# Kernel tuning notes

Hardware: AMD Instinct MI355X
Metric: run time of the kernel (lower is better)

## Reference

```python
import jax, jax.numpy as jnp
import numpy as np

N, F, H, OUT, DDIM, E = 200000, 64, 256, 16, 768, 3200000


def setup_inputs() -> dict:
    key = jax.random.key(0)
    ks = jax.random.split(key, 20)
    s = lambda i, shp, sc=0.05: (jax.random.normal(ks[i], shp, jnp.float32) * sc)
    return dict(
        x=jax.random.normal(ks[0], (N, F), jnp.float32),
        edge_index=jax.random.randint(ks[1], (2, E), 0, N, dtype=jnp.int32),
        doc_feature=jax.random.normal(ks[2], (DDIM,), jnp.float32),
        pool_w=s(3, (F,)),
        init_weight=s(4, (F, F)),
        gru_w_ih=s(5, (3 * F, F)), gru_w_hh=s(6, (3 * F, F)),
        gru_b_ih=s(7, (3 * F,)), gru_b_hh=s(8, (3 * F,)),
        gnn_fc_w=s(9, (H, F)), gnn_fc_b=s(10, (H,)),
        doc_fc_w=s(11, (H, DDIM)), doc_fc_b=s(12, (H,)),
        ln_g=jnp.ones((2 * H,), jnp.float32), ln_b=jnp.zeros((2 * H,), jnp.float32),
        fusion_w=s(13, (H, 2 * H)), fusion_b=s(14, (H,)),
        task_w=s(15, (OUT, H)), task_b=s(16, (OUT,)),
        time_w=s(17, (1, H)), time_b=s(18, (1,)),
    )


def _forward(x, doc_feature, pool_w, init_weight, gru_w_ih, gru_w_hh, gru_b_ih,
             gru_b_hh, gnn_fc_w, gnn_fc_b, doc_fc_w, doc_fc_b, ln_g, ln_b,
             fusion_w, fusion_b, task_w, task_b, time_w, time_b, edge_index):
    n, f = x.shape
    # --- EvolveGCNH: TopK pooling, k = f since ratio = in_channels/num_nodes ---
    score = x @ pool_w / jnp.linalg.norm(pool_w)             # [n]
    top_s, perm = jax.lax.top_k(score, f)
    x_tilde = x[perm] * jnp.tanh(top_s)[:, None]             # [f, f]
    # --- single-step GRU; hidden state = previous GCN weight (detached) ---
    h0 = jax.lax.stop_gradient(init_weight)                  # [f, f]
    gx = x_tilde @ gru_w_ih.T + gru_b_ih                     # [f, 3f]
    gh = h0 @ gru_w_hh.T + gru_b_hh
    xr, xz, xn = jnp.split(gx, 3, axis=1)
    hr, hz, hn = jnp.split(gh, 3, axis=1)
    r = jax.nn.sigmoid(xr + hr)
    z = jax.nn.sigmoid(xz + hz)
    nc = jnp.tanh(xn + r * hn)
    W = (1.0 - z) * nc + z * h0                              # evolved weight [f, f]
    # --- GCNConv with fixed W: sym-norm adjacency with self loops ---
    xw = x @ W                                               # [n, f]
    loop = jnp.arange(n, dtype=edge_index.dtype)
    row = jnp.concatenate([edge_index[0], loop])
    col = jnp.concatenate([edge_index[1], loop])
    deg = jax.ops.segment_sum(jnp.ones_like(col, dtype=x.dtype), col, num_segments=n)
    dis = jnp.where(deg > 0, jax.lax.rsqrt(jnp.maximum(deg, 1e-12)), 0.0)
    norm = dis[row] * dis[col]                               # [E+n]
    x_gnn = jax.ops.segment_sum(xw[row] * norm[:, None], col, num_segments=n)  # [n, f]
    # --- global mean pool (batch is all zeros -> single graph) ---
    pooled = jnp.mean(x_gnn, axis=0, keepdims=True)          # [1, f]
    g = pooled @ gnn_fc_w.T + gnn_fc_b                        # [1, H]
    d = jax.nn.relu(doc_feature @ doc_fc_w.T + doc_fc_b)[None, :]  # [1, H]
    fused = jnp.concatenate([g, d], axis=1)                   # [1, 2H]
    mu = jnp.mean(fused, axis=-1, keepdims=True)
    var = jnp.var(fused, axis=-1, keepdims=True)
    ln = (fused - mu) * jax.lax.rsqrt(var + 1e-5) * ln_g + ln_b
    h1 = jax.nn.relu(ln @ fusion_w.T + fusion_b)              # dropout = identity (eval)
    return (h1 @ task_w.T + task_b, h1 @ time_w.T + time_b)


def reference(x, edge_index, doc_feature, pool_w, init_weight, gru_w_ih, gru_w_hh,
              gru_b_ih, gru_b_hh, gnn_fc_w, gnn_fc_b, doc_fc_w, doc_fc_b, ln_g,
              ln_b, fusion_w, fusion_b, task_w, task_b, time_w, time_b):
    return _forward(x, doc_feature, pool_w, init_weight, gru_w_ih, gru_w_hh,
                    gru_b_ih, gru_b_hh, gnn_fc_w, gnn_fc_b, doc_fc_w, doc_fc_b,
                    ln_g, ln_b, fusion_w, fusion_b, task_w, task_b, time_w,
                    time_b, edge_index)
```

## Files before the change

### kernel.cpp

```cpp
#include <hip/hip_runtime.h>
#include <hip/hip_bf16.h>

#define NN    200000
#define EE    3200000
#define DDIMC 768

#define NI4   800000
#define HTH   1024
#define PARTW (25 * 12 * 8192)

#define BSZC  32768
#define BSHC  15
#define NBC   7
#define CCC   72
#define DEGC  (NBC * (BSZC / 2))
#define BSZR  16384
#define BSHR  14
#define NBR   13
#define CCR   40
#define PARTC (NBR * BSZR)

#define NDBLK 782
#define XBLOCKS 1024
#define CAPL  4096

#define HB    64
#define HW    32768

#define P_PART  0
#define P_DEGM  0
#define P_PARTM 0
#define ZLEN1   (8 * DEGC)
#define ZLEN2   (8 * PARTC)
#define P_HIST  PARTW
#define P_CANDN (P_HIST + 65536)
#define P_S8    (P_CANDN + 8)
#define ZERO_LEN (8 + 512)
#define P_FLAG  (P_S8 + 512)
#define P_THR   (P_FLAG + 8)
#define P_SV    (P_THR + 8)
#define P_D     (P_SV + 64)
#define P_DIS   (P_D + 256)
#define P_C     (P_DIS + NN)
#define P_SCORE (P_C + NN)
#define P_CKEY  (P_SCORE + NN)
#define P_CIDX  (P_CKEY + 4096)
#define P_XT    (P_CIDX + 4096)
#define P_WW    (P_XT + 4096)
#define P_G     (P_WW + 4096)
#define P_LNV   (P_G + 256)
#define P_H1    (P_LNV + 512)

__device__ __forceinline__ float ldf(const void* p, int i, int bf) {
  if (bf) return __bfloat162float(((const __hip_bfloat16*)p)[i]);
  return ((const float*)p)[i];
}
__device__ __forceinline__ void stf(void* p, int i, float v, int bf) {
  if (bf) ((__hip_bfloat16*)p)[i] = __float2bfloat16(v);
  else ((float*)p)[i] = v;
}
__device__ __forceinline__ float bfu(unsigned u) {
  return __uint_as_float(u << 16);
}
__device__ __forceinline__ float wsum(float v) {
#pragma unroll
  for (int m = 32; m >= 1; m >>= 1) v += __shfl_xor(v, m, 64);
  return v;
}
__device__ __forceinline__ int wsumi(int v) {
#pragma unroll
  for (int m = 32; m >= 1; m >>= 1) v += __shfl_xor(v, m, 64);
  return v;
}
__device__ __forceinline__ unsigned sortkey(float f) {
  unsigned u = __float_as_uint(f);
  return (u & 0x80000000u) ? ~u : (u | 0x80000000u);
}

__global__ void k_detect(const unsigned short* x16, int* flag) {
  __shared__ int cnt;
  if (threadIdx.x == 0) cnt = 0;
  __syncthreads();
  int ok = 0;
  for (int k = threadIdx.x; k < 512; k += 256) {
    unsigned short u = x16[2 * k];
    int e = (u >> 7) & 0xFF;
    if (u == 0 || (e >= 100 && e <= 150)) ok++;
  }
  atomicAdd(&cnt, ok);
  __syncthreads();
  if (threadIdx.x == 0) flag[0] = (cnt >= 400) ? 1 : 0;
}

__global__ void __launch_bounds__(HTH) k_hcol(const int* __restrict__ col,
                                              unsigned* __restrict__ degm) {
  __shared__ unsigned lh[BSZC / 2];
  int t = threadIdx.x;
  int b = blockIdx.x / CCC, j = blockIdx.x % CCC;
  for (int k = t; k < BSZC / 2; k += HTH) lh[k] = 0u;
  __syncthreads();
  int base = b << BSHC;
  const int4* c4 = (const int4*)col;
  const int stride = CCC * HTH;
  for (int i = j * HTH + t; i < NI4; i += 2 * stride) {
    int4 v0 = c4[i];
    int i2 = i + stride;
    int4 v1; v1.x = v1.y = v1.z = v1.w = -1;
    if (i2 < NI4) v1 = c4[i2];
    {
      int a0 = v0.x - base, a1 = v0.y - base, a2 = v0.z - base, a3 = v0.w - base;
      if ((unsigned)a0 < (unsigned)BSZC) atomicAdd(&lh[a0 >> 1], 1u << ((a0 & 1) * 16));
      if ((unsigned)a1 < (unsigned)BSZC) atomicAdd(&lh[a1 >> 1], 1u << ((a1 & 1) * 16));
      if ((unsigned)a2 < (unsigned)BSZC) atomicAdd(&lh[a2 >> 1], 1u << ((a2 & 1) * 16));
      if ((unsigned)a3 < (unsigned)BSZC) atomicAdd(&lh[a3 >> 1], 1u << ((a3 & 1) * 16));
    }
    {
      int a0 = v1.x - base, a1 = v1.y - base, a2 = v1.z - base, a3 = v1.w - base;
      if ((unsigned)a0 < (unsigned)BSZC) atomicAdd(&lh[a0 >> 1], 1u << ((a0 & 1) * 16));
      if ((unsigned)a1 < (unsigned)BSZC) atomicAdd(&lh[a1 >> 1], 1u << ((a1 & 1) * 16));
      if ((unsigned)a2 < (unsigned)BSZC) atomicAdd(&lh[a2 >> 1], 1u << ((a2 & 1) * 16));
      if ((unsigned)a3 < (unsigned)BSZC) atomicAdd(&lh[a3 >> 1], 1u << ((a3 & 1) * 16));
    }
  }
  __syncthreads();
  unsigned* dst = degm + (size_t)(j & 7) * DEGC + (size_t)b * (BSZC / 2);
  for (int k = t; k < BSZC / 2; k += HTH) {
    unsigned v = lh[k];
    if (v) atomicAdd(&dst[k], v);
  }
}

__global__ void k_redA(const unsigned* __restrict__ degm, float* __restrict__ dis,
                       const void* docf, const void* dw, const void* db,
                       float* __restrict__ d, const int* flagp) {
  if (blockIdx.x < NDBLK) {
    int i = blockIdx.x * 256 + threadIdx.x;
    if (i < NN) {
      int sh = (i & 1) * 16;
      int deg = 1;
#pragma unroll
      for (int p = 0; p < 8; p++) {
        unsigned w_ = degm[(size_t)p * DEGC + (i >> 1)];
        deg += (int)((w_ >> sh) & 0xffffu);
      }
      dis[i] = rsqrtf((float)deg);
    }
  } else {
    int flag = flagp[0];
    int o = (blockIdx.x - NDBLK) * 4 + (threadIdx.x >> 6);
    int lane = threadIdx.x & 63;
    float acc = 0.f;
    for (int k = lane; k < DDIMC; k += 64) acc += ldf(docf, k, flag) * ldf(dw, o * DDIMC + k, flag);
    acc = wsum(acc);
    if (lane == 0) d[o] = fmaxf(acc + ldf(db, o, flag), 0.0f);
  }
}

__global__ void __launch_bounds__(HTH) k_hrow(const int* __restrict__ row, const int* __restrict__ col,
                                              const float* __restrict__ dis,
                                              float* __restrict__ partm) {
  __shared__ float lh[BSZR];
  int t = threadIdx.x;
  int b = blockIdx.x / CCR, j = blockIdx.x % CCR;
  for (int k = t; k < BSZR; k += HTH) lh[k] = 0.f;
  __syncthreads();
  int base = b << BSHR;
  const int4* r4 = (const int4*)row;
  const int4* c4 = (const int4*)col;
  const int stride = CCR * HTH;
  for (int i = j * HTH + t; i < NI4; i += 2 * stride) {
    int4 r0 = r4[i];
    int4 c0 = c4[i];
    int i2 = i + stride;
    int4 r1; r1.x = r1.y = r1.z = r1.w = -1;
    int4 c1; c1.x = c1.y = c1.z = c1.w = 0;
    if (i2 < NI4) { r1 = r4[i2]; c1 = c4[i2]; }
    {
      int a0 = r0.x - base, a1 = r0.y - base, a2 = r0.z - base, a3 = r0.w - base;
      if ((unsigned)a0 < (unsigned)BSZR) atomicAdd(&lh[a0], dis[c0.x]);
      if ((unsigned)a1 < (unsigned)BSZR) atomicAdd(&lh[a1], dis[c0.y]);
      if ((unsigned)a2 < (unsigned)BSZR) atomicAdd(&lh[a2], dis[c0.z]);
      if ((unsigned)a3 < (unsigned)BSZR) atomicAdd(&lh[a3], dis[c0.w]);
    }
    {
      int a0 = r1.x - base, a1 = r1.y - base, a2 = r1.z - base, a3 = r1.w - base;
      if ((unsigned)a0 < (unsigned)BSZR) atomicAdd(&lh[a0], dis[c1.x]);
      if ((unsigned)a1 < (unsigned)BSZR) atomicAdd(&lh[a1], dis[c1.y]);
      if ((unsigned)a2 < (unsigned)BSZR) atomicAdd(&lh[a2], dis[c1.z]);
      if ((unsigned)a3 < (unsigned)BSZR) atomicAdd(&lh[a3], dis[c1.w]);
    }
  }
  __syncthreads();
  float* dst = partm + (size_t)(j & 7) * PARTC + (size_t)b * BSZR;
  for (int k = t; k < BSZR; k += HTH) {
    float v = lh[k];
    if (v != 0.f) atomicAdd(&dst[k], v);
  }
}

__global__ void k_redB(const float* __restrict__ partm, const float* __restrict__ dis,
                       float* __restrict__ c) {
  int i = blockIdx.x * 256 + threadIdx.x;
  if (i < NN) {
    float s = 0.f;
#pragma unroll
    for (int p = 0; p < 8; p++) s += partm[(size_t)p * PARTC + i];
    float dv = dis[i];
    c[i] = dv * s + dv * dv;
  }
}

__global__ void k_x(const void* x, const void* pw, const float* __restrict__ c,
                    float* __restrict__ score,
                    float* __restrict__ s8, const int* flagp) {
  __shared__ float sred[4][64];
  int flag = flagp[0];
  int t = threadIdx.x;
  int lane = t & 63;
  int w = t >> 6;
  int wid = (blockIdx.x * 256 + t) >> 6;
  int nw = (gridDim.x * 256) >> 6;

  if (flag) {
    int g  = lane >> 3;
    int c0 = (lane & 7) * 8;
    float pwv[8];
#pragma unroll
    for (int j = 0; j < 8; j++) pwv[j] = ldf(pw, c0 + j, 1);
    float s = 0.f;
#pragma unroll
    for (int j = 0; j < 8; j++) s += pwv[j] * pwv[j];
    float inv = 1.0f / sqrtf(wsum(s) * 0.125f);
    float sacc[8] = {0.f, 0.f, 0.f, 0.f, 0.f, 0.f, 0.f, 0.f};
    const uint4* x4 = (const uint4*)x;
    for (int r0 = wid * 8; r0 < NN; r0 += nw * 8) {
      int r = r0 + g;
      uint4 u = x4[r * 8 + (lane & 7)];
      float xv[8] = { bfu(u.x & 0xffff), bfu(u.x >> 16),
                      bfu(u.y & 0xffff), bfu(u.y >> 16),
                      bfu(u.z & 0xffff), bfu(u.z >> 16),
                      bfu(u.w & 0xffff), bfu(u.w >> 16) };
      float dot = 0.f;
#pragma unroll
      for (int j = 0; j < 8; j++) dot += xv[j] * pwv[j];
      dot += __shfl_xor(dot, 1, 64);
      dot += __shfl_xor(dot, 2, 64);
      dot += __shfl_xor(dot, 4, 64);
      float cr = c[r];
#pragma unroll
      for (int j = 0; j < 8; j++) sacc[j] += cr * xv[j];
      if ((lane & 7) == 0) score[r] = dot * inv;
    }
#pragma unroll
    for (int j = 0; j < 8; j++) {
      sacc[j] += __shfl_xor(sacc[j], 8, 64);
      sacc[j] += __shfl_xor(sacc[j], 16, 64);
      sacc[j] += __shfl_xor(sacc[j], 32, 64);
    }
    if (lane < 8) {
#pragma unroll
      for (int j = 0; j < 8; j++) sred[w][lane * 8 + j] = sacc[j];
    }
  } else {
    int g  = lane >> 4;
    int c0 = (lane & 15) * 4;
    float pwv[4];
#pragma unroll
    for (int j = 0; j < 4; j++) pwv[j] = ((const float*)pw)[c0 + j];
    float s = 0.f;
#pragma unroll
    for (int j = 0; j < 4; j++) s += pwv[j] * pwv[j];
    float inv = 1.0f / sqrtf(wsum(s) * (1.f / 16.f));
    float sacc[4] = {0.f, 0.f, 0.f, 0.f};
    const float4* x4 = (const float4*)x;
    for (int r0 = wid * 4; r0 < NN; r0 += nw * 4) {
      int r = r0 + g;
      float4 v = x4[r * 16 + (lane & 15)];
      float xv[4] = { v.x, v.y, v.z, v.w };
      float dot = 0.f;
#pragma unroll
      for (int j = 0; j < 4; j++) dot += xv[j] * pwv[j];
      dot += __shfl_xor(dot, 1, 64);
      dot += __shfl_xor(dot, 2, 64);
      dot += __shfl_xor(dot, 4, 64);
      dot += __shfl_xor(dot, 8, 64);
      float cr = c[r];
#pragma unroll
      for (int j = 0; j < 4; j++) sacc[j] += cr * xv[j];
      if ((lane & 15) == 0) score[r] = dot * inv;
    }
#pragma unroll
    for (int j = 0; j < 4; j++) {
      sacc[j] += __shfl_xor(sacc[j], 16, 64);
      sacc[j] += __shfl_xor(sacc[j], 32, 64);
    }
    if (lane < 16) {
#pragma unroll
      for (int j = 0; j < 4; j++) sred[w][lane * 4 + j] = sacc[j];
    }
  }
  __syncthreads();
  if (w == 0)
    atomicAdd(&s8[(blockIdx.x & 7) * 64 + lane],
              sred[0][lane] + sred[1][lane] + sred[2][lane] + sred[3][lane]);
}

__global__ void __launch_bounds__(1024) k_hist(const float* __restrict__ score,
                                               unsigned* __restrict__ part) {
  __shared__ unsigned lh[HW];
  int t = threadIdx.x;
  for (int k = t; k < HW; k += 1024) lh[k] = 0u;
  __syncthreads();
  int r0 = blockIdx.x * (NN / HB);
  int r1 = r0 + (NN / HB);
  for (int i = r0 + t; i < r1; i += 1024) {
    unsigned b = sortkey(score[i]) >> 16;
    atomicAdd(&lh[b >> 1], 1u << ((b & 1) * 16));
  }
  __syncthreads();
  unsigned* dst = part + (size_t)blockIdx.x * HW;
  for (int k = t; k < HW; k += 1024) dst[k] = lh[k];
}

__global__ void k_redH(const unsigned* __restrict__ part, int* __restrict__ hist) {
  int w = blockIdx.x * 256 + threadIdx.x;
  unsigned lo = 0, hi = 0;
  for (int b = 0; b < HB; b++) {
    unsigned v = part[(size_t)b * HW + w];
    lo += v & 0xffffu;
    hi += v >> 16;
  }
  hist[2 * w]     = (int)lo;
  hist[2 * w + 1] = (int)hi;
}

__global__ void k_thresh(const int* __restrict__ hist, int* __restrict__ thrB,
                         const float* __restrict__ s8, float* __restrict__ svec) {
  __shared__ int part[256];
  __shared__ int segl[256];
  __shared__ int res2[2];
  int t = threadIdx.x, w = t >> 6, lane = t & 63;
  if (t < 64) {
    float a = 0.f;
    for (int r = 0; r < 8; r++) a += s8[r * 64 + t];
    svec[t] = a;
  }
  for (int m = w; m < 256; m += 4) {
    const int* hb = &hist[m * 256];
    int a = hb[lane] + hb[lane + 64] + hb[lane + 128] + hb[lane + 192];
    a = wsumi(a);
    if (lane == 0) part[m] = a;
  }
  __syncthreads();
  if (t == 0) {
    int acc = 0, seg = 0, above = 0;
    for (int b = 255; b >= 0; b--) {
      if (acc + part[b] >= 64) { seg = b; above = acc; break; }
      acc += part[b];
    }
    res2[0] = seg; res2[1] = above;
  }
  __syncthreads();
  segl[t] = hist[res2[0] * 256 + t];
  __syncthreads();
  if (t == 0) {
    int acc = res2[1], B = res2[0] * 256;
    for (int j = 255; j >= 0; j--) {
      acc += segl[j];
      if (acc >= 64) { B = res2[0] * 256 + j; break; }
    }
    thrB[0] = B;
  }
}

__global__ void k_collect(const float* __restrict__ score, const int* __restrict__ thrB,
                          int* __restrict__ candn, unsigned* __restrict__ ckey,
                          int* __restrict__ cidx) {
  int i = blockIdx.x * blockDim.x + threadIdx.x;
  if (i >= NN) return;
  unsigned u = sortkey(score[i]);
  if ((int)(u >> 16) >= thrB[0]) {
    int p = atomicAdd(candn, 1);
    if (p < CAPL) { ckey[p] = u; cidx[p] = i; }
  }
}

__global__ void __launch_bounds__(1024) k_top(const int* __restrict__ candn,
                      const unsigned* __restrict__ ckey,
                      const int* __restrict__ cidx, const void* x,
                      float* __restrict__ xt, const int* flagp) {
  __shared__ unsigned long long keys[CAPL];
  __shared__ int perm[64];
  __shared__ float ts[64];
  int flag = flagp[0];
  int t = threadIdx.x;
  int M = candn[0];
  if (M > CAPL) M = CAPL;
  for (int j = t; j < M; j += 1024)
    keys[j] = (((unsigned long long)ckey[j]) << 32) |
              (unsigned long long)(0xFFFFFFFFu - (unsigned)cidx[j]);
  __syncthreads();
  for (int j = t; j < M; j += 1024) {
    unsigned long long k = keys[j];
    int rank = 0;
    for (int i = 0; i < M; i++) rank += (keys[i] > k) ? 1 : 0;
    if (rank < 64) {
      unsigned ku = (unsigned)(k >> 32);
      unsigned idx = 0xFFFFFFFFu - (unsigned)(k & 0xFFFFFFFFu);
      perm[rank] = (int)idx;
      unsigned bits = (ku & 0x80000000u) ? (ku ^ 0x80000000u) : ~ku;
      ts[rank] = tanhf(__uint_as_float(bits));
    }
  }
  __syncthreads();
  for (int q = t; q < 4096; q += 1024) {
    int j = q >> 6, f = q & 63;
    xt[q] = ldf(x, perm[j] * 64 + f, flag) * ts[j];
  }
}

#define GS 193
__device__ __forceinline__ void stage_w(const void* src, float* dst, int flag, int t) {
  if (flag) {
    const uint4* s4 = (const uint4*)src;
    for (int k = t; k < 1536; k += 256) {
      uint4 u = s4[k];
      int e = k << 3; int o = e >> 6, f = e & 63;
      float* d = &dst[f * GS + o];
      d[0]      = bfu(u.x & 0xffff); d[GS]     = bfu(u.x >> 16);
      d[2 * GS] = bfu(u.y & 0xffff); d[3 * GS] = bfu(u.y >> 16);
      d[4 * GS] = bfu(u.z & 0xffff); d[5 * GS] = bfu(u.z >> 16);
      d[6 * GS] = bfu(u.w & 0xffff); d[7 * GS] = bfu(u.w >> 16);
    }
  } else {
    const float4* s4 = (const float4*)src;
    for (int k = t; k < 3072; k += 256) {
      float4 v = s4[k];
      int e = k << 2; int o = e >> 6, f = e & 63;
      float* d = &dst[f * GS + o];
      d[0] = v.x; d[GS] = v.y; d[2 * GS] = v.z; d[3 * GS] = v.w;
    }
  }
}

__global__ void k_gru(const float* __restrict__ xt, const void* h0g, const void* wihg,
                      const void* whhg, const void* bihg, const void* bhhg,
                      float* __restrict__ Wout, const int* flagp) {
  __shared__ float wb1[64 * GS];
  __shared__ float wb2[64 * GS];
  __shared__ float xtr[256];
  __shared__ float h0r[256];
  int flag = flagp[0];
  int t = threadIdx.x;
  int j0 = blockIdx.x * 4;
  { int jj = t >> 6, f = t & 63;
    xtr[t] = xt[(j0 + jj) * 64 + f];
    h0r[t] = ldf(h0g, (j0 + jj) * 64 + f, flag); }
  stage_w(wihg, wb1, flag, t);
  stage_w(whhg, wb2, flag, t);
  __syncthreads();
  int jl = t >> 6, c2 = t & 63;
  float xr = 0, xz = 0, xn = 0, hr = 0, hz = 0, hn = 0;
#pragma unroll 4
  for (int f = 0; f < 64; f++) {
    float xv = xtr[jl * 64 + f];
    float hv = h0r[jl * 64 + f];
    const float* w1 = &wb1[f * GS];
    const float* w2 = &wb2[f * GS];
    xr += xv * w1[c2]; xz += xv * w1[64 + c2]; xn += xv * w1[128 + c2];
    hr += hv * w2[c2]; hz += hv * w2[64 + c2]; hn += hv * w2[128 + c2];
  }
  xr += ldf(bihg, c2, flag); xz += ldf(bihg, 64 + c2, flag); xn += ldf(bihg, 128 + c2, flag);
  hr += ldf(bhhg, c2, flag); hz += ldf(bhhg, 64 + c2, flag); hn += ldf(bhhg, 128 + c2, flag);
  float rg = 1.f / (1.f + expf(-(xr + hr)));
  float zg = 1.f / (1.f + expf(-(xz + hz)));
  float nc = tanhf(xn + rg * hn);
  Wout[(j0 + jl) * 64 + c2] = (1.f - zg) * nc + zg * h0r[jl * 64 + c2];
}

__global__ void k_g(const float* __restrict__ svec, const float* __restrict__ Wm,
                    const void* gw, const void* gb, float* __restrict__ g,
                    const int* flagp) {
  __shared__ float pooled[64];
  int flag = flagp[0];
  int t = threadIdx.x, w = t >> 6, lane = t & 63;
  if (t < 64) {
    float a = 0.f;
    for (int f = 0; f < 64; f++) a += svec[f] * Wm[f * 64 + t];
    pooled[t] = a * (1.0f / (float)NN);
  }
  __syncthreads();
  int o = blockIdx.x * 4 + w;
  float acc = pooled[lane] * ldf(gw, o * 64 + lane, flag);
  acc = wsum(acc);
  if (lane == 0) g[o] = acc + ldf(gb, o, flag);
}

__global__ void k_ln(const float* __restrict__ g, const float* __restrict__ d,
                     const void* lng, const void* lnb, float* __restrict__ lnv,
                     const int* flagp) {
  __shared__ float red[256];
  __shared__ float stats[2];
  int flag = flagp[0];
  int t = threadIdx.x;
  float v0 = g[t], v1 = d[t];
  red[t] = v0 + v1; __syncthreads();
  for (int s = 128; s > 0; s >>= 1) { if (t < s) red[t] += red[t + s]; __syncthreads(); }
  if (t == 0) stats[0] = red[0];
  __syncthreads();
  red[t] = v0 * v0 + v1 * v1; __syncthreads();
  for (int s = 128; s > 0; s >>= 1) { if (t < s) red[t] += red[t + s]; __syncthreads(); }
  if (t == 0) stats[1] = red[0];
  __syncthreads();
  float mu = stats[0] * (1.f / 512.f);
  float var = stats[1] * (1.f / 512.f) - mu * mu;
  float istd = rsqrtf(var + 1e-5f);
  lnv[t]       = (v0 - mu) * istd * ldf(lng, t, flag)       + ldf(lnb, t, flag);
  lnv[t + 256] = (v1 - mu) * istd * ldf(lng, t + 256, flag) + ldf(lnb, t + 256, flag);
}

__global__ void k_fuse(const float* __restrict__ lnv, const void* fw, const void* fb,
                       float* __restrict__ h1, const int* flagp) {
  __shared__ float lv[512];
  int flag = flagp[0];
  int t = threadIdx.x, w = t >> 6, lane = t & 63;
  lv[t] = lnv[t]; lv[t + 256] = lnv[t + 256];
  __syncthreads();
  int o = blockIdx.x * 4 + w;
  float acc = 0.f;
  if (flag) {
    uint4 u = *((const uint4*)((const unsigned short*)fw + o * 512) + lane);
    const float* l = &lv[lane * 8];
    acc = bfu(u.x & 0xffff) * l[0] + bfu(u.x >> 16) * l[1]
        + bfu(u.y & 0xffff) * l[2] + bfu(u.y >> 16) * l[3]
        + bfu(u.z & 0xffff) * l[4] + bfu(u.z >> 16) * l[5]
        + bfu(u.w & 0xffff) * l[6] + bfu(u.w >> 16) * l[7];
  } else {
    const float4* fv = (const float4*)((const float*)fw + o * 512);
    float4 a = fv[lane * 2], b = fv[lane * 2 + 1];
    const float* l = &lv[lane * 8];
    acc = a.x * l[0] + a.y * l[1] + a.z * l[2] + a.w * l[3]
        + b.x * l[4] + b.y * l[5] + b.z * l[6] + b.w * l[7];
  }
  acc = wsum(acc);
  if (lane == 0) h1[o] = fmaxf(acc + ldf(fb, o, flag), 0.0f);
}

__global__ void k_out(const float* __restrict__ h1, const void* tw, const void* tb,
                      const void* tmw, const void* tmb, void* out, const int* flagp) {
  int flag = flagp[0];
  int t = threadIdx.x, w = t >> 6, lane = t & 63;
  int o = blockIdx.x * 4 + w;
  if (o >= 17) return;
  float acc = 0.f;
  if (o < 16) { for (int k = lane; k < 256; k += 64) acc += h1[k] * ldf(tw, o * 256 + k, flag); }
  else        { for (int k = lane; k < 256; k += 64) acc += h1[k] * ldf(tmw, k, flag); }
  acc = wsum(acc);
  if (lane == 0) {
    float bias = (o < 16) ? ldf(tb, o, flag) : ldf(tmb, 0, flag);
    stf(out, o, acc + bias, flag);
  }
}

extern "C" void kernel_launch(void* const* d_in, const int* in_sizes, int n_in,
                              void* d_out, int out_size, void* d_ws, size_t ws_size,
                              hipStream_t stream) {
  const void* x    = d_in[0];
  const int*  ei   = (const int*)d_in[1];
  const void* docf = d_in[2];
  const void* pw   = d_in[3];
  const void* h0   = d_in[4];
  const void* wih  = d_in[5];
  const void* whh  = d_in[6];
  const void* bih  = d_in[7];
  const void* bhh  = d_in[8];
  const void* gw   = d_in[9];
  const void* gb   = d_in[10];
  const void* dw   = d_in[11];
  const void* db   = d_in[12];
  const void* lng  = d_in[13];
  const void* lnb  = d_in[14];
  const void* fw   = d_in[15];
  const void* fb   = d_in[16];
  const void* tw   = d_in[17];
  const void* tb   = d_in[18];
  const void* tmw  = d_in[19];
  const void* tmb  = d_in[20];

  const int* row = ei;
  const int* col = ei + EE;

  float* wsf = (float*)d_ws;
  int*   wsi = (int*)d_ws;

  hipMemsetAsync(wsi + P_DEGM, 0, (size_t)ZLEN1 * 4, stream);
  hipMemsetAsync(wsi + P_CANDN, 0, (size_t)ZERO_LEN * 4, stream);
  k_detect<<<1, 256, 0, stream>>>((const unsigned short*)x, wsi + P_FLAG);
  k_hcol<<<NBC * CCC, HTH, 0, stream>>>(col, (unsigned*)(wsi + P_DEGM));
  k_redA<<<NDBLK + 64, 256, 0, stream>>>((const unsigned*)(wsi + P_DEGM), wsf + P_DIS,
                                         docf, dw, db, wsf + P_D, wsi + P_FLAG);
  hipMemsetAsync(wsi + P_PARTM, 0, (size_t)ZLEN2 * 4, stream);
  k_hrow<<<NBR * CCR, HTH, 0, stream>>>(row, col, wsf + P_DIS, wsf + P_PARTM);
  k_redB<<<NDBLK, 256, 0, stream>>>(wsf + P_PARTM, wsf + P_DIS, wsf + P_C);
  k_x<<<XBLOCKS, 256, 0, stream>>>(x, pw, wsf + P_C, wsf + P_SCORE,
                                   wsf + P_S8, wsi + P_FLAG);
  k_hist<<<HB, 1024, 0, stream>>>(wsf + P_SCORE, (unsigned*)(wsi + P_PART));
  k_redH<<<HW / 256, 256, 0, stream>>>((const unsigned*)(wsi + P_PART), wsi + P_HIST);
  k_thresh<<<1, 256, 0, stream>>>(wsi + P_HIST, wsi + P_THR, wsf + P_S8, wsf + P_SV);
  k_collect<<<NDBLK, 256, 0, stream>>>(wsf + P_SCORE, wsi + P_THR, wsi + P_CANDN,
                                       (unsigned*)(wsi + P_CKEY), wsi + P_CIDX);
  k_top<<<1, 1024, 0, stream>>>(wsi + P_CANDN, (const unsigned*)(wsi + P_CKEY),
                                wsi + P_CIDX, x, wsf + P_XT, wsi + P_FLAG);
  k_gru<<<16, 256, 0, stream>>>(wsf + P_XT, h0, wih, whh, bih, bhh, wsf + P_WW, wsi + P_FLAG);
  k_g<<<64, 256, 0, stream>>>(wsf + P_SV, wsf + P_WW, gw, gb, wsf + P_G, wsi + P_FLAG);
  k_ln<<<1, 256, 0, stream>>>(wsf + P_G, wsf + P_D, lng, lnb, wsf + P_LNV, wsi + P_FLAG);
  k_fuse<<<64, 256, 0, stream>>>(wsf + P_LNV, fw, fb, wsf + P_H1, wsi + P_FLAG);
  k_out<<<5, 256, 0, stream>>>(wsf + P_H1, tw, tb, tmw, tmb, d_out, wsi + P_FLAG);
}
```

Before: 325.3 us.

## Write per-block histogram partitions and reduce them instead of atomic merging

Adds variants of the degree and row-sum histogram kernels where each block stores its shared-memory histogram to a private slot in workspace, followed by reduction kernels summing over slots. This removes the zeroing memsets and global atomic merges when workspace is large enough, selected at runtime by workspace size. In exchange it writes and rereads tens of megabytes of partial histograms, which may cost more bandwidth than the atomics it replaces.

```diff
diff --git a/kernel.cpp b/kernel.cpp
--- a/kernel.cpp
+++ b/kernel.cpp
@@ -27,29 +27,9 @@
 #define HB    64
 #define HW    32768
 
-#define P_PART  0
-#define P_DEGM  0
-#define P_PARTM 0
 #define ZLEN1   (8 * DEGC)
 #define ZLEN2   (8 * PARTC)
-#define P_HIST  PARTW
-#define P_CANDN (P_HIST + 65536)
-#define P_S8    (P_CANDN + 8)
-#define ZERO_LEN (8 + 512)
-#define P_FLAG  (P_S8 + 512)
-#define P_THR   (P_FLAG + 8)
-#define P_SV    (P_THR + 8)
-#define P_D     (P_SV + 64)
-#define P_DIS   (P_D + 256)
-#define P_C     (P_DIS + NN)
-#define P_SCORE (P_C + NN)
-#define P_CKEY  (P_SCORE + NN)
-#define P_CIDX  (P_CKEY + 4096)
-#define P_XT    (P_CIDX + 4096)
-#define P_WW    (P_XT + 4096)
-#define P_G     (P_WW + 4096)
-#define P_LNV   (P_G + 256)
-#define P_H1    (P_LNV + 512)
+#define BIGPART (CCR * NBR * BSZR)
 
 __device__ __forceinline__ float ldf(const void* p, int i, int bf) {
   if (bf) return __bfloat162float(((const __hip_bfloat16*)p)[i]);
@@ -90,6 +70,124 @@
   atomicAdd(&cnt, ok);
   __syncthreads();
   if (threadIdx.x == 0) flag[0] = (cnt >= 400) ? 1 : 0;
+}
+
+
+__global__ void __launch_bounds__(HTH) k_hcolB(const int* __restrict__ col,
+                                               unsigned* __restrict__ part) {
+  __shared__ unsigned lh[BSZC / 2];
+  int t = threadIdx.x;
+  int b = blockIdx.x / CCC, j = blockIdx.x % CCC;
+  for (int k = t; k < BSZC / 2; k += HTH) lh[k] = 0u;
+  __syncthreads();
+  int base = b << BSHC;
+  const int4* c4 = (const int4*)col;
+  const int stride = CCC * HTH;
+  for (int i = j * HTH + t; i < NI4; i += 2 * stride) {
+    int4 v0 = c4[i];
+    int i2 = i + stride;
+    int4 v1; v1.x = v1.y = v1.z = v1.w = -1;
+    if (i2 < NI4) v1 = c4[i2];
+    {
+      int a0 = v0.x - base, a1 = v0.y - base, a2 = v0.z - base, a3 = v0.w - base;
+      if ((unsigned)a0 < (unsigned)BSZC) atomicAdd(&lh[a0 >> 1], 1u << ((a0 & 1) * 16));
+      if ((unsigned)a1 < (unsigned)BSZC) atomicAdd(&lh[a1 >> 1], 1u << ((a1 & 1) * 16));
+      if ((unsigned)a2 < (unsigned)BSZC) atomicAdd(&lh[a2 >> 1], 1u << ((a2 & 1) * 16));
+      if ((unsigned)a3 < (unsigned)BSZC) atomicAdd(&lh[a3 >> 1], 1u << ((a3 & 1) * 16));
+    }
+    {
+      int a0 = v1.x - base, a1 = v1.y - base, a2 = v1.z - base, a3 = v1.w - base;
+      if ((unsigned)a0 < (unsigned)BSZC) atomicAdd(&lh[a0 >> 1], 1u << ((a0 & 1) * 16));
+      if ((unsigned)a1 < (unsigned)BSZC) atomicAdd(&lh[a1 >> 1], 1u << ((a1 & 1) * 16));
+      if ((unsigned)a2 < (unsigned)BSZC) atomicAdd(&lh[a2 >> 1], 1u << ((a2 & 1) * 16));
+      if ((unsigned)a3 < (unsigned)BSZC) atomicAdd(&lh[a3 >> 1], 1u << ((a3 & 1) * 16));
+    }
+  }
+  __syncthreads();
+  unsigned* dst = part + (size_t)blockIdx.x * (BSZC / 2);
+  for (int k = 4 * t; k < BSZC / 2; k += 4 * HTH)
+    *(uint4*)&dst[k] = *(const uint4*)&lh[k];
+}
+
+__global__ void k_redAB(const unsigned* __restrict__ part, float* __restrict__ dis,
+                        const void* docf, const void* dw, const void* db,
+                        float* __restrict__ d, const int* flagp) {
+  if (blockIdx.x < NDBLK) {
+    int i = blockIdx.x * 256 + threadIdx.x;
+    if (i < NN) {
+      int b = i >> BSHC;
+      int k = (i & (BSZC - 1)) >> 1;
+      const unsigned* p = part + (size_t)b * CCC * (BSZC / 2) + k;
+      unsigned s = 0;
+#pragma unroll 8
+      for (int j = 0; j < CCC; j++) s += p[(size_t)j * (BSZC / 2)];
+      int deg = 1 + (int)((s >> ((i & 1) * 16)) & 0xffffu);
+      dis[i] = rsqrtf((float)deg);
+    }
+  } else {
+    int flag = flagp[0];
+    int o = (blockIdx.x - NDBLK) * 4 + (threadIdx.x >> 6);
+    int lane = threadIdx.x & 63;
+    float acc = 0.f;
+    for (int k = lane; k < DDIMC; k += 64) acc += ldf(docf, k, flag) * ldf(dw, o * DDIMC + k, flag);
+    acc = wsum(acc);
+    if (lane == 0) d[o] = fmaxf(acc + ldf(db, o, flag), 0.0f);
+  }
+}
+
+__global__ void __launch_bounds__(HTH) k_hrowB(const int* __restrict__ row, const int* __restrict__ col,
+                                               const float* __restrict__ dis,
+                                               float* __restrict__ part) {
+  __shared__ float lh[BSZR];
+  int t = threadIdx.x;
+  int b = blockIdx.x / CCR, j = blockIdx.x % CCR;
+  for (int k = t; k < BSZR; k += HTH) lh[k] = 0.f;
+  __syncthreads();
+  int base = b << BSHR;
+  const int4* r4 = (const int4*)row;
+  const int4* c4 = (const int4*)col;
+  const int stride = CCR * HTH;
+  for (int i = j * HTH + t; i < NI4; i += 2 * stride) {
+    int4 r0 = r4[i];
+    int4 c0 = c4[i];
+    int i2 = i + stride;
+    int4 r1; r1.x = r1.y = r1.z = r1.w = -1;
+    int4 c1; c1.x = c1.y = c1.z = c1.w = 0;
+    if (i2 < NI4) { r1 = r4[i2]; c1 = c4[i2]; }
+    {
+      int a0 = r0.x - base, a1 = r0.y - base, a2 = r0.z - base, a3 = r0.w - base;
+      if ((unsigned)a0 < (unsigned)BSZR) atomicAdd(&lh[a0], dis[c0.x]);
+      if ((unsigned)a1 < (unsigned)BSZR) atomicAdd(&lh[a1], dis[c0.y]);
+      if ((unsigned)a2 < (unsigned)BSZR) atomicAdd(&lh[a2], dis[c0.z]);
+      if ((unsigned)a3 < (unsigned)BSZR) atomicAdd(&lh[a3], dis[c0.w]);
+    }
+    {
+      int a0 = r1.x - base, a1 = r1.y - base, a2 = r1.z - base, a3 = r1.w - base;
+      if ((unsigned)a0 < (unsigned)BSZR) atomicAdd(&lh[a0], dis[c1.x]);
+      if ((unsigned)a1 < (unsigned)BSZR) atomicAdd(&lh[a1], dis[c1.y]);
+      if ((unsigned)a2 < (unsigned)BSZR) atomicAdd(&lh[a2], dis[c1.z]);
+      if ((unsigned)a3 < (unsigned)BSZR) atomicAdd(&lh[a3], dis[c1.w]);
+    }
+  }
+  __syncthreads();
+  float* dst = part + (size_t)blockIdx.x * BSZR;
+  for (int k = 4 * t; k < BSZR; k += 4 * HTH)
+    *(float4*)&dst[k] = *(const float4*)&lh[k];
+}
+
+__global__ void k_redBB(const float* __restrict__ part, const float* __restrict__ dis,
+                        float* __restrict__ c) {
+  int i = blockIdx.x * 256 + threadIdx.x;
+  if (i < NN) {
+    int b = i >> BSHR;
+    int k = i & (BSZR - 1);
+    const float* p = part + (size_t)b * CCR * BSZR + k;
+    float s = 0.f;
+#pragma unroll 8
+    for (int j = 0; j < CCR; j++) s += p[(size_t)j * BSZR];
+    float dv = dis[i];
+    c[i] = dv * s + dv * dv;
+  }
 }
 
 __global__ void __launch_bounds__(HTH) k_hcol(const int* __restrict__ col,
@@ -593,27 +691,58 @@
   float* wsf = (float*)d_ws;
   int*   wsi = (int*)d_ws;
 
-  hipMemsetAsync(wsi + P_DEGM, 0, (size_t)ZLEN1 * 4, stream);
-  hipMemsetAsync(wsi + P_CANDN, 0, (size_t)ZERO_LEN * 4, stream);
-  k_detect<<<1, 256, 0, stream>>>((const unsigned short*)x, wsi + P_FLAG);
-  k_hcol<<<NBC * CCC, HTH, 0, stream>>>(col, (unsigned*)(wsi + P_DEGM));
-  k_redA<<<NDBLK + 64, 256, 0, stream>>>((const unsigned*)(wsi + P_DEGM), wsf + P_DIS,
-                                         docf, dw, db, wsf + P_D, wsi + P_FLAG);
-  hipMemsetAsync(wsi + P_PARTM, 0, (size_t)ZLEN2 * 4, stream);
-  k_hrow<<<NBR * CCR, HTH, 0, stream>>>(row, col, wsf + P_DIS, wsf + P_PARTM);
-  k_redB<<<NDBLK, 256, 0, stream>>>(wsf + P_PARTM, wsf + P_DIS, wsf + P_C);
-  k_x<<<XBLOCKS, 256, 0, stream>>>(x, pw, wsf + P_C, wsf + P_SCORE,
-                                   wsf + P_S8, wsi + P_FLAG);
-  k_hist<<<HB, 1024, 0, stream>>>(wsf + P_SCORE, (unsigned*)(wsi + P_PART));
-  k_redH<<<HW / 256, 256, 0, stream>>>((const unsigned*)(wsi + P_PART), wsi + P_HIST);
-  k_thresh<<<1, 256, 0, stream>>>(wsi + P_HIST, wsi + P_THR, wsf + P_S8, wsf + P_SV);
-  k_collect<<<NDBLK, 256, 0, stream>>>(wsf + P_SCORE, wsi + P_THR, wsi + P_CANDN,
-                                       (unsigned*)(wsi + P_CKEY), wsi + P_CIDX);
-  k_top<<<1, 1024, 0, stream>>>(wsi + P_CANDN, (const unsigned*)(wsi + P_CKEY),
-                                wsi + P_CIDX, x, wsf + P_XT, wsi + P_FLAG);
-  k_gru<<<16, 256, 0, stream>>>(wsf + P_XT, h0, wih, whh, bih, bhh, wsf + P_WW, wsi + P_FLAG);
-  k_g<<<64, 256, 0, stream>>>(wsf + P_SV, wsf + P_WW, gw, gb, wsf + P_G, wsi + P_FLAG);
-  k_ln<<<1, 256, 0, stream>>>(wsf + P_G, wsf + P_D, lng, lnb, wsf + P_LNV, wsi + P_FLAG);
-  k_fuse<<<64, 256, 0, stream>>>(wsf + P_LNV, fw, fb, wsf + P_H1, wsi + P_FLAG);
-  k_out<<<5, 256, 0, stream>>>(wsf + P_H1, tw, tb, tmw, tmb, d_out, wsi + P_FLAG);
-}
+  int big = (ws_size >= (size_t)42 * 1024 * 1024);
+  size_t base = big ? (size_t)BIGPART : (size_t)PARTW;
+
+  size_t oHIST  = base;
+  size_t oCANDN = oHIST + 65536;
+  size_t oS8    = oCANDN + 8;
+  size_t oFLAG  = oS8 + 512;
+  size_t oTHR   = oFLAG + 8;
+  size_t oSV    = oTHR + 8;
+  size_t oD     = oSV + 64;
+  size_t oDIS   = oD + 256;
+  size_t oC     = oDIS + NN;
+  size_t oSCORE = oC + NN;
+  size_t oCKEY  = oSCORE + NN;
+  size_t oCIDX  = oCKEY + 4096;
+  size_t oXT    = oCIDX + 4096;
+  size_t oWW    = oXT + 4096;
+  size_t oG     = oWW + 4096;
+  size_t oLNV   = oG + 256;
+  size_t oH1    = oLNV + 512;
+
+  hipMemsetAsync(wsi + oCANDN, 0, (size_t)(8 + 512) * 4, stream);
+  k_detect<<<1, 256, 0, stream>>>((const unsigned short*)x, wsi + oFLAG);
+
+  if (big) {
+    k_hcolB<<<NBC * CCC, HTH, 0, stream>>>(col, (unsigned*)wsi);
+    k_redAB<<<NDBLK + 64, 256, 0, stream>>>((const unsigned*)wsi, wsf + oDIS,
+                                            docf, dw, db, wsf + oD, wsi + oFLAG);
+    k_hrowB<<<NBR * CCR, HTH, 0, stream>>>(row, col, wsf + oDIS, wsf);
+    k_redBB<<<NDBLK, 256, 0, stream>>>(wsf, wsf + oDIS, wsf + oC);
+  } else {
+    hipMemsetAsync(wsi, 0, (size_t)ZLEN1 * 4, stream);
+    k_hcol<<<NBC * CCC, HTH, 0, stream>>>(col, (unsigned*)wsi);
+    k_redA<<<NDBLK + 64, 256, 0, stream>>>((const unsigned*)wsi, wsf + oDIS,
+                                           docf, dw, db, wsf + oD, wsi + oFLAG);
+    hipMemsetAsync(wsi, 0, (size_t)ZLEN2 * 4, stream);
+    k_hrow<<<NBR * CCR, HTH, 0, stream>>>(row, col, wsf + oDIS, wsf);
+    k_redB<<<NDBLK, 256, 0, stream>>>(wsf, wsf + oDIS, wsf + oC);
+  }
+
+  k_x<<<XBLOCKS, 256, 0, stream>>>(x, pw, wsf + oC, wsf + oSCORE,
+                                   wsf + oS8, wsi + oFLAG);
+  k_hist<<<HB, 1024, 0, stream>>>(wsf + oSCORE, (unsigned*)wsi);
+  k_redH<<<HW / 256, 256, 0, stream>>>((const unsigned*)wsi, wsi + oHIST);
+  k_thresh<<<1, 256, 0, stream>>>(wsi + oHIST, wsi + oTHR, wsf + oS8, wsf + oSV);
+  k_collect<<<NDBLK, 256, 0, stream>>>(wsf + oSCORE, wsi + oTHR, wsi + oCANDN,
+                                       (unsigned*)(wsi + oCKEY), wsi + oCIDX);
+  k_top<<<1, 1024, 0, stream>>>(wsi + oCANDN, (const unsigned*)(wsi + oCKEY),
+                                wsi + oCIDX, x, wsf + oXT, wsi + oFLAG);
+  k_gru<<<16, 256, 0, stream>>>(wsf + oXT, h0, wih, whh, bih, bhh, wsf + oWW, wsi + oFLAG);
+  k_g<<<64, 256, 0, stream>>>(wsf + oSV, wsf + oWW, gw, gb, wsf + oG, wsi + oFLAG);
+  k_ln<<<1, 256, 0, stream>>>(wsf + oG, wsf + oD, lng, lnb, wsf + oLNV, wsi + oFLAG);
+  k_fuse<<<64, 256, 0, stream>>>(wsf + oLNV, fw, fb, wsf + oH1, wsi + oFLAG);
+  k_out<<<5, 256, 0, stream>>>(wsf + oH1, tw, tb, tmw, tmb, d_out, wsi + oFLAG);
+}
```

Result: faster. 308.3 us (-5.2%).
